# Kernel tuning notes

Measured on AMD Instinct MI355X. Metric: run time of the kernel, lower is better.

The kernel has to match this reference:

```python
import jax, jax.numpy as jnp
import numpy as np

B, T, D = 4, 8192, 512
N_LEVELS = 3
N_HEAD = 4
HEAD_DIM = D // N_HEAD
STRIDES = (8, 4, 4)
SEGS = (T // 8, T // 32, T // 128)  # 1024, 256, 64 segments per level
LN_EPS = 1e-5


def setup_inputs() -> dict:
    key = jax.random.key(0)
    ks = jax.random.split(key, 8)
    h_bytes = jax.random.normal(ks[0], (B, T, D), jnp.float32)
    def strided_boundaries(length, stride):
        b = np.zeros((B, length), np.int32)
        b[:, ::stride] = 1  # segment-start markers; first position always a boundary
        return jnp.asarray(b)
    b0 = strided_boundaries(T, STRIDES[0])
    b1 = strided_boundaries(SEGS[0], STRIDES[1])
    b2 = strided_boundaries(SEGS[1], STRIDES[2])
    s = 0.02
    return dict(
        h_bytes=h_bytes, b0=b0, b1=b1, b2=b2,
        mlp_ln_g=jnp.ones((N_LEVELS, D), jnp.float32),
        mlp_ln_b=jnp.zeros((N_LEVELS, D), jnp.float32),
        mlp_w1=jax.random.normal(ks[1], (N_LEVELS, D, 2 * D), jnp.float32) * s,
        mlp_b1=jnp.zeros((N_LEVELS, 2 * D), jnp.float32),
        mlp_w2=jax.random.normal(ks[2], (N_LEVELS, 2 * D, D), jnp.float32) * s,
        mlp_b2=jnp.zeros((N_LEVELS, D), jnp.float32),
        # 8 linears per cross-level block: bu_q,bu_k,bu_v,bu_out,td_q,td_k,td_v,td_out
        ca_w=jax.random.normal(ks[3], (N_LEVELS - 1, 8, D, D), jnp.float32) * s,
        ca_b=jnp.zeros((N_LEVELS - 1, 8, D), jnp.float32),
        ca_ln_g=jnp.ones((N_LEVELS - 1, 2, D), jnp.float32),  # [.,0]=bu_norm, [.,1]=td_norm
        ca_ln_b=jnp.zeros((N_LEVELS - 1, 2, D), jnp.float32),
    )


def _ln(x, g, b):
    mu = jnp.mean(x, axis=-1, keepdims=True)
    xc = x - mu
    var = jnp.mean(xc * xc, axis=-1, keepdims=True)
    return xc * jax.lax.rsqrt(var + LN_EPS) * g + b


def _mha(xq, xkv, Wq, Wk, Wv, Wo, bq, bk, bv, bo):
    Bq, Sq, _ = xq.shape
    Skv = xkv.shape[1]
    q = (xq @ Wq + bq).reshape(Bq, Sq, N_HEAD, HEAD_DIM)
    k = (xkv @ Wk + bk).reshape(Bq, Skv, N_HEAD, HEAD_DIM)
    v = (xkv @ Wv + bv).reshape(Bq, Skv, N_HEAD, HEAD_DIM)
    scores = jnp.einsum('bqhd,bkhd->bhqk', q, k) * (1.0 / (HEAD_DIM ** 0.5))
    att = jax.nn.softmax(scores, axis=-1)
    out = jnp.einsum('bhqk,bkhd->bqhd', att, v).reshape(Bq, Sq, D)
    return out @ Wo + bo


def _segment_mean_pool(x, seg_ids, n_seg):
    # x: [B, T, D], seg_ids: [B, T] in [0, n_seg)
    sums = jax.vmap(lambda xi, si: jax.ops.segment_sum(xi, si, num_segments=n_seg))(x, seg_ids)
    cnts = jax.vmap(lambda si: jax.ops.segment_sum(jnp.ones(si.shape, jnp.float32), si, num_segments=n_seg))(seg_ids)
    return sums / jnp.maximum(cnts, 1.0)[..., None]


def reference(h_bytes, b0, b1, b2, mlp_ln_g, mlp_ln_b, mlp_w1, mlp_b1, mlp_w2, mlp_b2, ca_w, ca_b, ca_ln_g, ca_ln_b):
    bounds = (b0, b1, b2)
    segs = []
    cur = h_bytes
    for lvl in range(N_LEVELS):
        seg_ids = jnp.cumsum(bounds[lvl], axis=1) - 1  # boundary marks segment start
        pooled = _segment_mean_pool(cur, seg_ids, SEGS[lvl])
        h = _ln(pooled, mlp_ln_g[lvl], mlp_ln_b[lvl])
        h = jax.nn.gelu(h @ mlp_w1[lvl] + mlp_b1[lvl], approximate=False)
        pooled = pooled + (h @ mlp_w2[lvl] + mlp_b2[lvl])
        segs.append(pooled)
        cur = pooled
    # top-down cross-level refinement
    for i in range(N_LEVELS - 2, -1, -1):
        fine, coarse = segs[i], segs[i + 1]
        fn = _ln(fine, ca_ln_g[i, 0], ca_ln_b[i, 0])
        fu = fine + _mha(fn, coarse, ca_w[i, 0], ca_w[i, 1], ca_w[i, 2], ca_w[i, 3],
                         ca_b[i, 0], ca_b[i, 1], ca_b[i, 2], ca_b[i, 3])
        cn = _ln(coarse, ca_ln_g[i, 1], ca_ln_b[i, 1])
        cu = coarse + _mha(cn, fu, ca_w[i, 4], ca_w[i, 5], ca_w[i, 6], ca_w[i, 7],
                           ca_b[i, 4], ca_b[i, 5], ca_b[i, 6], ca_b[i, 7])
        segs[i], segs[i + 1] = fu, cu
    return tuple(segs)
```

## Files before the change

### kernel.cpp

```cpp
#include <hip/hip_runtime.h>
#include <hip/hip_bf16.h>
#include <math.h>

#define NHEAD 4

typedef __attribute__((ext_vector_type(8))) short bf16x8;
typedef __attribute__((ext_vector_type(4))) float f32x4;
typedef unsigned short u16;

__device__ __forceinline__ u16 f2b(float f) {
  unsigned u = __float_as_uint(f);
  u = u + 0x7fffu + ((u >> 16) & 1u);
  return (u16)(u >> 16);
}
__device__ __forceinline__ float gelu_exact(float x) {
  return 0.5f * x * (1.0f + erff(x * 0.70710678118654752f));
}

__global__ __launch_bounds__(1024) void scan_bounds_kernel(
    const int* __restrict__ bnd, int* __restrict__ starts, int n, int nseg) {
  __shared__ int sums[1024];
  int row = blockIdx.x;
  const int* br = bnd + (size_t)row * n;
  int chunk = (n + 1023) / 1024;
  int t0 = threadIdx.x * chunk;
  int t1 = t0 + chunk; if (t1 > n) t1 = n;
  int s = 0;
  for (int t = t0; t < t1; ++t) s += br[t];
  sums[threadIdx.x] = s;
  __syncthreads();
  for (int off = 1; off < 1024; off <<= 1) {
    int v = (threadIdx.x >= off) ? sums[threadIdx.x - off] : 0;
    __syncthreads();
    sums[threadIdx.x] += v;
    __syncthreads();
  }
  int run = sums[threadIdx.x] - s;
  for (int t = t0; t < t1; ++t) {
    if (br[t]) { starts[(size_t)row * nseg + run] = t; ++run; }
  }
}

__global__ __launch_bounds__(128) void pool_kernel(
    const float* __restrict__ x, const int* __restrict__ starts,
    float* __restrict__ y, int Tin, int nseg) {
  int s = blockIdx.x, b = blockIdx.y;
  int st = starts[(size_t)b * nseg + s];
  int en = (s + 1 < nseg) ? starts[(size_t)b * nseg + s + 1] : Tin;
  const float* xb = x + (size_t)b * Tin * 512;
  int d = threadIdx.x * 4;
  float4 acc = make_float4(0.f, 0.f, 0.f, 0.f);
  for (int t = st; t < en; ++t) {
    float4 v = *(const float4*)(xb + (size_t)t * 512 + d);
    acc.x += v.x; acc.y += v.y; acc.z += v.z; acc.w += v.w;
  }
  int cnt = en - st; if (cnt < 1) cnt = 1;
  float inv = 1.0f / (float)cnt;
  *(float4*)(y + ((size_t)b * nseg + s) * 512 + d) =
      make_float4(acc.x * inv, acc.y * inv, acc.z * inv, acc.w * inv);
}

__global__ __launch_bounds__(256) void ln_kernel(
    const float* __restrict__ x, const float* __restrict__ g,
    const float* __restrict__ bt, u16* __restrict__ y, int ntok) {
  int wave = threadIdx.x >> 6, lane = threadIdx.x & 63;
  int tok = blockIdx.x * 4 + wave;
  if (tok >= ntok) return;
  const float* xr = x + (size_t)tok * 512;
  int d = lane * 8;
  float4 v0 = *(const float4*)(xr + d);
  float4 v1 = *(const float4*)(xr + d + 4);
  float s = v0.x + v0.y + v0.z + v0.w + v1.x + v1.y + v1.z + v1.w;
  #pragma unroll
  for (int off = 32; off; off >>= 1) s += __shfl_xor(s, off, 64);
  float mean = s * (1.0f / 512.0f);
  float a[8] = {v0.x-mean, v0.y-mean, v0.z-mean, v0.w-mean,
                v1.x-mean, v1.y-mean, v1.z-mean, v1.w-mean};
  float ss = 0.f;
  #pragma unroll
  for (int i = 0; i < 8; ++i) ss += a[i]*a[i];
  #pragma unroll
  for (int off = 32; off; off >>= 1) ss += __shfl_xor(ss, off, 64);
  float inv = rsqrtf(ss * (1.0f / 512.0f) + 1e-5f);
  float4 g0 = *(const float4*)(g + d), g1 = *(const float4*)(g + d + 4);
  float4 b0 = *(const float4*)(bt + d), b1 = *(const float4*)(bt + d + 4);
  float gg[8] = {g0.x,g0.y,g0.z,g0.w,g1.x,g1.y,g1.z,g1.w};
  float bb[8] = {b0.x,b0.y,b0.z,b0.w,b1.x,b1.y,b1.z,b1.w};
  union { u16 u[8]; uint4 v; } pk;
  #pragma unroll
  for (int i = 0; i < 8; ++i) pk.u[i] = f2b(a[i] * inv * gg[i] + bb[i]);
  *(uint4*)(y + (size_t)tok * 512 + d) = pk.v;
}

__global__ __launch_bounds__(256) void castbf_kernel(
    const float* __restrict__ x, u16* __restrict__ y, int n8) {
  int i = blockIdx.x * 256 + threadIdx.x;
  if (i >= n8) return;
  float4 v0 = *(const float4*)(x + (size_t)i * 8);
  float4 v1 = *(const float4*)(x + (size_t)i * 8 + 4);
  float a[8] = {v0.x,v0.y,v0.z,v0.w,v1.x,v1.y,v1.z,v1.w};
  union { u16 u[8]; uint4 v; } pk;
  #pragma unroll
  for (int j = 0; j < 8; ++j) pk.u[j] = f2b(a[j]);
  *(uint4*)(y + (size_t)i * 8) = pk.v;
}

__global__ __launch_bounds__(256) void wtrans_kernel(
    const float* __restrict__ W, u16* __restrict__ Wt, int K, int M) {
  __shared__ float tile[32][33];
  int m0 = blockIdx.x * 32, k0 = blockIdx.y * 32;
  const float* Wz = W + (size_t)blockIdx.z * K * M;
  u16* Wtz = Wt + (size_t)blockIdx.z * K * M;
  int x = threadIdx.x & 31, y = threadIdx.x >> 5;
  #pragma unroll
  for (int i = 0; i < 32; i += 8)
    tile[y + i][x] = Wz[(size_t)(k0 + y + i) * M + m0 + x];
  __syncthreads();
  #pragma unroll
  for (int i = 0; i < 32; i += 8)
    Wtz[(size_t)(m0 + y + i) * K + k0 + x] = f2b(tile[x][y + i]);
}

__global__ __launch_bounds__(256) void vtrans_kernel(
    const u16* __restrict__ vb, u16* __restrict__ vT, int Skv) {
  __shared__ u16 tile[32][33];
  int kv0 = blockIdx.x * 32, d0 = blockIdx.y * 32;
  int z = blockIdx.z, b = z >> 2, h = z & 3;
  const u16* src = vb + ((size_t)b * Skv) * 512 + h * 128;
  u16* dst = vT + (size_t)z * 128 * Skv;
  int x = threadIdx.x & 31, y = threadIdx.x >> 5;
  #pragma unroll
  for (int i = 0; i < 32; i += 8)
    tile[y + i][x] = src[(size_t)(kv0 + y + i) * 512 + d0 + x];
  __syncthreads();
  #pragma unroll
  for (int i = 0; i < 32; i += 8)
    dst[(size_t)(d0 + y + i) * Skv + kv0 + x] = tile[x][y + i];
}

__global__ __launch_bounds__(256) void softmax_kernel(
    const float* __restrict__ S, u16* __restrict__ P, int L) {
  int wave = threadIdx.x >> 6, lane = threadIdx.x & 63;
  int row = blockIdx.x * 4 + wave;
  const float* sr = S + (size_t)row * L;
  u16* pr = P + (size_t)row * L;
  const float scale = 0.08838834764831845f;
  float mx = -1e30f;
  for (int j = lane; j < L; j += 64) mx = fmaxf(mx, sr[j]);
  #pragma unroll
  for (int off = 32; off; off >>= 1) mx = fmaxf(mx, __shfl_xor(mx, off, 64));
  float e[16];
  int cnt = L >> 6;
  float sum = 0.f;
  for (int c = 0; c < cnt; ++c) {
    e[c] = __expf((sr[lane + (c << 6)] - mx) * scale);
    sum += e[c];
  }
  #pragma unroll
  for (int off = 32; off; off >>= 1) sum += __shfl_xor(sum, off, 64);
  float inv = 1.0f / sum;
  for (int c = 0; c < cnt; ++c) pr[lane + (c << 6)] = f2b(e[c] * inv);
}

__device__ __forceinline__ void mfma_core(
    const u16* __restrict__ A, int lda, const u16* __restrict__ Wt, int ldw,
    int K, u16* AsB, u16* WsB, f32x4 acc[2][2]) {
  int t = threadIdx.x;
  int lane = t & 63, wave = t >> 6;
  int wr = (wave >> 1) * 32, wc = (wave & 1) * 32;
  int lrow = t >> 3;
  int lseg = t & 7;
  int swz = (lseg * 16) ^ ((lrow & 7) << 4);
  const u16* Ap0 = A + (size_t)lrow * lda + lseg * 8;
  const u16* Ap1 = Ap0 + (size_t)32 * lda;
  const u16* Wp0 = Wt + (size_t)lrow * ldw + lseg * 8;
  const u16* Wp1 = Wp0 + (size_t)32 * ldw;
  for (int k0 = 0; k0 < K; k0 += 64) {
    uint4 a0 = *(const uint4*)(Ap0 + k0);
    uint4 a1 = *(const uint4*)(Ap1 + k0);
    uint4 w0 = *(const uint4*)(Wp0 + k0);
    uint4 w1 = *(const uint4*)(Wp1 + k0);
    __syncthreads();
    *(uint4*)((char*)AsB + lrow * 128 + swz) = a0;
    *(uint4*)((char*)AsB + (lrow + 32) * 128 + swz) = a1;
    *(uint4*)((char*)WsB + lrow * 128 + swz) = w0;
    *(uint4*)((char*)WsB + (lrow + 32) * 128 + swz) = w1;
    __syncthreads();
    #pragma unroll
    for (int ks = 0; ks < 2; ++ks) {
      bf16x8 af[2], bfr[2];
      #pragma unroll
      for (int mi = 0; mi < 2; ++mi) {
        int row = wr + mi * 16 + (lane & 15);
        int cb = (ks * 64 + ((lane >> 4) << 4)) ^ ((row & 7) << 4);
        af[mi] = *(const bf16x8*)((const char*)AsB + row * 128 + cb);
      }
      #pragma unroll
      for (int ni = 0; ni < 2; ++ni) {
        int row = wc + ni * 16 + (lane & 15);
        int cb = (ks * 64 + ((lane >> 4) << 4)) ^ ((row & 7) << 4);
        bfr[ni] = *(const bf16x8*)((const char*)WsB + row * 128 + cb);
      }
      #pragma unroll
      for (int mi = 0; mi < 2; ++mi)
        #pragma unroll
        for (int ni = 0; ni < 2; ++ni)
          acc[mi][ni] = __builtin_amdgcn_mfma_f32_16x16x32_bf16(
              af[mi], bfr[ni], acc[mi][ni], 0, 0, 0);
    }
  }
}

__global__ __launch_bounds__(256) void gemm_k(
    const u16* __restrict__ A, int lda, const u16* __restrict__ Wt, int ldw,
    int K, const float* __restrict__ bias, float* __restrict__ Cf,
    u16* __restrict__ Cb, int ldc, int flags) {
  __shared__ u16 As[4096], Ws[4096];
  int n0 = blockIdx.y * 64, m0 = blockIdx.x * 64;
  f32x4 acc[2][2];
  #pragma unroll
  for (int i = 0; i < 2; ++i)
    #pragma unroll
    for (int j = 0; j < 2; ++j) acc[i][j] = (f32x4){0.f, 0.f, 0.f, 0.f};
  mfma_core(A + (size_t)n0 * lda, lda, Wt + (size_t)m0 * ldw, ldw, K, As, Ws, acc);
  int lane = threadIdx.x & 63, wave = threadIdx.x >> 6;
  int wr = (wave >> 1) * 32, wc = (wave & 1) * 32;
  #pragma unroll
  for (int mi = 0; mi < 2; ++mi) {
    #pragma unroll
    for (int ni = 0; ni < 2; ++ni) {
      int col = m0 + wc + ni * 16 + (lane & 15);
      float bv = bias[col];
      #pragma unroll
      for (int j = 0; j < 4; ++j) {
        int row = n0 + wr + mi * 16 + ((lane >> 4) << 2) + j;
        float v = acc[mi][ni][j] + bv;
        if (flags & 1) v = gelu_exact(v);
        size_t idx = (size_t)row * ldc + col;
        if (flags & 2) v += Cf[idx];
        if (flags & 4) Cf[idx] = v;
        if (flags & 8) Cb[idx] = f2b(v);
      }
    }
  }
}

__global__ __launch_bounds__(256) void scores_k(
    const u16* __restrict__ Qb, const u16* __restrict__ Kb,
    float* __restrict__ S, int Sq, int Skv) {
  __shared__ u16 As[4096], Ws[4096];
  int z = blockIdx.z, b = z >> 2, h = z & 3;
  int n0 = blockIdx.y * 64, m0 = blockIdx.x * 64;
  const u16* Ap = Qb + ((size_t)b * Sq + n0) * 512 + h * 128;
  const u16* Wp = Kb + ((size_t)b * Skv + m0) * 512 + h * 128;
  f32x4 acc[2][2];
  #pragma unroll
  for (int i = 0; i < 2; ++i)
    #pragma unroll
    for (int j = 0; j < 2; ++j) acc[i][j] = (f32x4){0.f, 0.f, 0.f, 0.f};
  mfma_core(Ap, 512, Wp, 512, 128, As, Ws, acc);
  float* Sz = S + (size_t)z * Sq * Skv;
  int lane = threadIdx.x & 63, wave = threadIdx.x >> 6;
  int wr = (wave >> 1) * 32, wc = (wave & 1) * 32;
  #pragma unroll
  for (int mi = 0; mi < 2; ++mi)
    #pragma unroll
    for (int ni = 0; ni < 2; ++ni) {
      int col = m0 + wc + ni * 16 + (lane & 15);
      #pragma unroll
      for (int j = 0; j < 4; ++j) {
        int row = n0 + wr + mi * 16 + ((lane >> 4) << 2) + j;
        Sz[(size_t)row * Skv + col] = acc[mi][ni][j];
      }
    }
}

__global__ __launch_bounds__(256) void pv_k(
    const u16* __restrict__ P, const u16* __restrict__ vT,
    u16* __restrict__ O, int Sq, int Skv) {
  __shared__ u16 As[4096], Ws[4096];
  int z = blockIdx.z, b = z >> 2, h = z & 3;
  int n0 = blockIdx.y * 64, m0 = blockIdx.x * 64;
  const u16* Ap = P + (size_t)z * Sq * Skv + (size_t)n0 * Skv;
  const u16* Wp = vT + (size_t)z * 128 * Skv + (size_t)m0 * Skv;
  f32x4 acc[2][2];
  #pragma unroll
  for (int i = 0; i < 2; ++i)
    #pragma unroll
    for (int j = 0; j < 2; ++j) acc[i][j] = (f32x4){0.f, 0.f, 0.f, 0.f};
  mfma_core(Ap, Skv, Wp, Skv, Skv, As, Ws, acc);
  int lane = threadIdx.x & 63, wave = threadIdx.x >> 6;
  int wr = (wave >> 1) * 32, wc = (wave & 1) * 32;
  #pragma unroll
  for (int mi = 0; mi < 2; ++mi)
    #pragma unroll
    for (int ni = 0; ni < 2; ++ni) {
      int col = m0 + wc + ni * 16 + (lane & 15);
      #pragma unroll
      for (int j = 0; j < 4; ++j) {
        int row = n0 + wr + mi * 16 + ((lane >> 4) << 2) + j;
        O[((size_t)b * Sq + row) * 512 + h * 128 + col] = f2b(acc[mi][ni][j]);
      }
    }
}

extern "C" void kernel_launch(void* const* d_in, const int* in_sizes, int n_in,
                              void* d_out, int out_size, void* d_ws, size_t ws_size,
                              hipStream_t stream) {
  (void)in_sizes; (void)n_in; (void)out_size; (void)ws_size;
  const float* h_bytes  = (const float*)d_in[0];
  const int*   b0       = (const int*)d_in[1];
  const int*   b1       = (const int*)d_in[2];
  const int*   b2       = (const int*)d_in[3];
  const float* mlp_ln_g = (const float*)d_in[4];
  const float* mlp_ln_b = (const float*)d_in[5];
  const float* mlp_w1   = (const float*)d_in[6];
  const float* mlp_b1   = (const float*)d_in[7];
  const float* mlp_w2   = (const float*)d_in[8];
  const float* mlp_b2   = (const float*)d_in[9];
  const float* ca_w     = (const float*)d_in[10];
  const float* ca_b     = (const float*)d_in[11];
  const float* ca_ln_g  = (const float*)d_in[12];
  const float* ca_ln_b  = (const float*)d_in[13];

  float* out0 = (float*)d_out;
  float* out1 = out0 + 4 * 1024 * 512;
  float* out2 = out1 + 4 * 256 * 512;

  char* wsb = (char*)d_ws;
  u16* w1t = (u16*)wsb;
  u16* w2t = w1t + 3 * 524288;
  u16* cat = w2t + 3 * 524288;
  u16*   lnbuf = (u16*)(wsb + (14u << 20));
  u16*   hbuf  = (u16*)(wsb + (18u << 20));
  u16*   qb    = (u16*)(wsb + (18u << 20));
  u16*   kb    = (u16*)(wsb + (22u << 20));
  u16*   Pbuf  = (u16*)(wsb + (18u << 20));
  u16*   vT    = (u16*)(wsb + (26u << 20));
  u16*   vb    = (u16*)(wsb + (30u << 20));
  u16*   ccbf  = (u16*)(wsb + (34u << 20));
  float* Sbuf  = (float*)(wsb + (30u << 20));
  u16*   abuf  = (u16*)(wsb + (46u << 20));
  int* starts0 = (int*)(wsb + (50u << 20));
  int* starts1 = starts0 + 4096;
  int* starts2 = starts1 + 1024;

  wtrans_kernel<<<dim3(32, 16, 3), 256, 0, stream>>>(mlp_w1, w1t, 512, 1024);
  wtrans_kernel<<<dim3(16, 32, 3), 256, 0, stream>>>(mlp_w2, w2t, 1024, 512);
  wtrans_kernel<<<dim3(16, 16, 16), 256, 0, stream>>>(ca_w, cat, 512, 512);

  scan_bounds_kernel<<<4, 1024, 0, stream>>>(b0, starts0, 8192, 1024);
  scan_bounds_kernel<<<4, 1024, 0, stream>>>(b1, starts1, 1024, 256);
  scan_bounds_kernel<<<4, 1024, 0, stream>>>(b2, starts2, 256, 64);

  auto mlp = [&](float* X, int Ntok, int lvl) {
    ln_kernel<<<Ntok / 4, 256, 0, stream>>>(X, mlp_ln_g + lvl * 512,
                                            mlp_ln_b + lvl * 512, lnbuf, Ntok);
    gemm_k<<<dim3(16, Ntok / 64), 256, 0, stream>>>(
        lnbuf, 512, w1t + (size_t)lvl * 524288, 512, 512,
        mlp_b1 + lvl * 1024, nullptr, hbuf, 1024, 1 | 8);
    gemm_k<<<dim3(8, Ntok / 64), 256, 0, stream>>>(
        hbuf, 1024, w2t + (size_t)lvl * 524288, 1024, 1024,
        mlp_b2 + lvl * 512, X, nullptr, 512, 2 | 4);
  };
  pool_kernel<<<dim3(1024, 4), 128, 0, stream>>>(h_bytes, starts0, out0, 8192, 1024);
  mlp(out0, 4096, 0);
  pool_kernel<<<dim3(256, 4), 128, 0, stream>>>(out0, starts1, out1, 1024, 256);
  mlp(out1, 1024, 1);
  pool_kernel<<<dim3(64, 4), 128, 0, stream>>>(out1, starts2, out2, 256, 64);
  mlp(out2, 256, 2);

  auto cross = [&](int i, float* F, float* Cc, int nf, int nc) {
    u16* cw = cat + (size_t)i * 8 * 262144;
    const float* bb = ca_b + (size_t)i * 8 * 512;
    const float* lg = ca_ln_g + (size_t)i * 2 * 512;
    const float* lb = ca_ln_b + (size_t)i * 2 * 512;
    int Nf = 4 * nf, Nc = 4 * nc;
    ln_kernel<<<Nf / 4, 256, 0, stream>>>(F, lg, lb, lnbuf, Nf);
    gemm_k<<<dim3(8, Nf / 64), 256, 0, stream>>>(lnbuf, 512, cw, 512, 512,
                                                 bb, nullptr, qb, 512, 8);
    castbf_kernel<<<Nc / 4, 256, 0, stream>>>(Cc, ccbf, Nc * 64);
    gemm_k<<<dim3(8, Nc / 64), 256, 0, stream>>>(ccbf, 512, cw + 262144, 512, 512,
                                                 bb + 512, nullptr, kb, 512, 8);
    gemm_k<<<dim3(8, Nc / 64), 256, 0, stream>>>(ccbf, 512, cw + 2 * 262144, 512, 512,
                                                 bb + 1024, nullptr, vb, 512, 8);
    vtrans_kernel<<<dim3(nc / 32, 4, 16), 256, 0, stream>>>(vb, vT, nc);
    scores_k<<<dim3(nc / 64, nf / 64, 16), 256, 0, stream>>>(qb, kb, Sbuf, nf, nc);
    softmax_kernel<<<16 * nf / 4, 256, 0, stream>>>(Sbuf, Pbuf, nc);
    pv_k<<<dim3(2, nf / 64, 16), 256, 0, stream>>>(Pbuf, vT, abuf, nf, nc);
    gemm_k<<<dim3(8, Nf / 64), 256, 0, stream>>>(abuf, 512, cw + 3 * 262144, 512, 512,
                                                 bb + 3 * 512, F, nullptr, 512, 2 | 4);
    ln_kernel<<<Nc / 4, 256, 0, stream>>>(Cc, lg + 512, lb + 512, lnbuf, Nc);
    gemm_k<<<dim3(8, Nc / 64), 256, 0, stream>>>(lnbuf, 512, cw + 4 * 262144, 512, 512,
                                                 bb + 4 * 512, nullptr, qb, 512, 8);
    castbf_kernel<<<Nf / 4, 256, 0, stream>>>(F, ccbf, Nf * 64);
    gemm_k<<<dim3(8, Nf / 64), 256, 0, stream>>>(ccbf, 512, cw + 5 * 262144, 512, 512,
                                                 bb + 5 * 512, nullptr, kb, 512, 8);
    gemm_k<<<dim3(8, Nf / 64), 256, 0, stream>>>(ccbf, 512, cw + 6 * 262144, 512, 512,
                                                 bb + 6 * 512, nullptr, vb, 512, 8);
    vtrans_kernel<<<dim3(nf / 32, 4, 16), 256, 0, stream>>>(vb, vT, nf);
    scores_k<<<dim3(nf / 64, nc / 64, 16), 256, 0, stream>>>(qb, kb, Sbuf, nc, nf);
    softmax_kernel<<<16 * nc / 4, 256, 0, stream>>>(Sbuf, Pbuf, nf);
    pv_k<<<dim3(2, nc / 64, 16), 256, 0, stream>>>(Pbuf, vT, abuf, nc, nf);
    gemm_k<<<dim3(8, Nc / 64), 256, 0, stream>>>(abuf, 512, cw + 7 * 262144, 512, 512,
                                                 bb + 7 * 512, Cc, nullptr, 512, 2 | 4);
  };
  cross(1, out1, out2, 256, 64);
  cross(0, out0, out1, 1024, 256);
}
```

Before: 516.7 us.

## Fuse attention into flash kernel, merge launches, fuse pool+LN, prefetch GEMM tiles

Replaces the separate scores, softmax and PV kernels with a single fused attention kernel that keeps the scores on chip. The softmax skips the max subtraction and normalises once at the end. The pool and LayerNorm steps are fused into one kernel. The three weight-transpose launches and three scan launches are each merged into one. K and V projections are merged into a single wider GEMM, and the GEMM epilogues write bf16 mirrors so the cast kernels are no longer needed. The GEMM main loop gains register prefetch of the next K tile. Together these cut launches and HBM traffic for the score matrices, but dropping the max subtraction in softmax risks overflow when logits are large.

```diff
diff --git a/kernel.cpp b/kernel.cpp
--- a/kernel.cpp
+++ b/kernel.cpp
@@ -1,8 +1,6 @@
 #include <hip/hip_runtime.h>
 #include <hip/hip_bf16.h>
 #include <math.h>
-
-#define NHEAD 4
 
 typedef __attribute__((ext_vector_type(8))) short bf16x8;
 typedef __attribute__((ext_vector_type(4))) float f32x4;
@@ -17,14 +15,20 @@
   return 0.5f * x * (1.0f + erff(x * 0.70710678118654752f));
 }
 
-__global__ __launch_bounds__(1024) void scan_bounds_kernel(
-    const int* __restrict__ bnd, int* __restrict__ starts, int n, int nseg) {
+__global__ __launch_bounds__(1024) void scan_all_k(
+    const int* __restrict__ b0, const int* __restrict__ b1,
+    const int* __restrict__ b2, int* __restrict__ starts) {
   __shared__ int sums[1024];
-  int row = blockIdx.x;
-  const int* br = bnd + (size_t)row * n;
+  int lvl = blockIdx.y, row = blockIdx.x;
+  const int* bp = (lvl == 0) ? b0 : (lvl == 1) ? b1 : b2;
+  int n = (lvl == 0) ? 8192 : (lvl == 1) ? 1024 : 256;
+  int nseg = (lvl == 0) ? 1024 : (lvl == 1) ? 256 : 64;
+  int* sp = starts + ((lvl == 0) ? 0 : (lvl == 1) ? 4096 : 5120);
+  const int* br = bp + (size_t)row * n;
   int chunk = (n + 1023) / 1024;
   int t0 = threadIdx.x * chunk;
   int t1 = t0 + chunk; if (t1 > n) t1 = n;
+  if (t0 > n) t0 = n;
   int s = 0;
   for (int t = t0; t < t1; ++t) s += br[t];
   sums[threadIdx.x] = s;
@@ -37,27 +41,85 @@
   }
   int run = sums[threadIdx.x] - s;
   for (int t = t0; t < t1; ++t) {
-    if (br[t]) { starts[(size_t)row * nseg + run] = t; ++run; }
-  }
-}
-
-__global__ __launch_bounds__(128) void pool_kernel(
+    if (br[t]) { sp[(size_t)row * nseg + run] = t; ++run; }
+  }
+}
+
+__global__ __launch_bounds__(256) void wtrans_all_k(
+    const float* __restrict__ w1, const float* __restrict__ w2,
+    const float* __restrict__ ca, u16* __restrict__ w1t,
+    u16* __restrict__ w2t, u16* __restrict__ cat) {
+  __shared__ float tile[32][33];
+  int z = blockIdx.x;
+  const float* W; u16* Wt; int K, M, m0, k0;
+  if (z < 1536) {
+    int mat = z >> 9, tl = z & 511;
+    W = w1 + (size_t)mat * 524288; Wt = w1t + (size_t)mat * 524288;
+    K = 512; M = 1024; m0 = (tl & 31) * 32; k0 = (tl >> 5) * 32;
+  } else if (z < 3072) {
+    z -= 1536; int mat = z >> 9, tl = z & 511;
+    W = w2 + (size_t)mat * 524288; Wt = w2t + (size_t)mat * 524288;
+    K = 1024; M = 512; m0 = (tl & 15) * 32; k0 = (tl >> 4) * 32;
+  } else {
+    z -= 3072; int mat = z >> 8, tl = z & 255;
+    W = ca + (size_t)mat * 262144; Wt = cat + (size_t)mat * 262144;
+    K = 512; M = 512; m0 = (tl & 15) * 32; k0 = (tl >> 4) * 32;
+  }
+  int x = threadIdx.x & 31, y = threadIdx.x >> 5;
+  #pragma unroll
+  for (int i = 0; i < 32; i += 8)
+    tile[y + i][x] = W[(size_t)(k0 + y + i) * M + m0 + x];
+  __syncthreads();
+  #pragma unroll
+  for (int i = 0; i < 32; i += 8)
+    Wt[(size_t)(m0 + y + i) * K + k0 + x] = f2b(tile[x][y + i]);
+}
+
+__global__ __launch_bounds__(256) void pool_ln_k(
     const float* __restrict__ x, const int* __restrict__ starts,
-    float* __restrict__ y, int Tin, int nseg) {
-  int s = blockIdx.x, b = blockIdx.y;
+    float* __restrict__ pooled, const float* __restrict__ g,
+    const float* __restrict__ bt, u16* __restrict__ lnout,
+    int Tin, int nseg) {
+  int wv = threadIdx.x >> 6, lane = threadIdx.x & 63;
+  int s = blockIdx.x * 4 + wv, b = blockIdx.y;
   int st = starts[(size_t)b * nseg + s];
   int en = (s + 1 < nseg) ? starts[(size_t)b * nseg + s + 1] : Tin;
-  const float* xb = x + (size_t)b * Tin * 512;
-  int d = threadIdx.x * 4;
-  float4 acc = make_float4(0.f, 0.f, 0.f, 0.f);
+  const float* xb = x + ((size_t)b * Tin) * 512;
+  int d = lane * 8;
+  float a[8] = {0.f,0.f,0.f,0.f,0.f,0.f,0.f,0.f};
   for (int t = st; t < en; ++t) {
-    float4 v = *(const float4*)(xb + (size_t)t * 512 + d);
-    acc.x += v.x; acc.y += v.y; acc.z += v.z; acc.w += v.w;
+    const float* row = xb + (size_t)t * 512 + d;
+    float4 v0 = *(const float4*)row;
+    float4 v1 = *(const float4*)(row + 4);
+    a[0]+=v0.x; a[1]+=v0.y; a[2]+=v0.z; a[3]+=v0.w;
+    a[4]+=v1.x; a[5]+=v1.y; a[6]+=v1.z; a[7]+=v1.w;
   }
   int cnt = en - st; if (cnt < 1) cnt = 1;
-  float inv = 1.0f / (float)cnt;
-  *(float4*)(y + ((size_t)b * nseg + s) * 512 + d) =
-      make_float4(acc.x * inv, acc.y * inv, acc.z * inv, acc.w * inv);
+  float ic = 1.0f / (float)cnt;
+  #pragma unroll
+  for (int i = 0; i < 8; ++i) a[i] *= ic;
+  int tok = b * nseg + s;
+  float* pr = pooled + (size_t)tok * 512 + d;
+  *(float4*)pr = make_float4(a[0], a[1], a[2], a[3]);
+  *(float4*)(pr + 4) = make_float4(a[4], a[5], a[6], a[7]);
+  float sm = a[0]+a[1]+a[2]+a[3]+a[4]+a[5]+a[6]+a[7];
+  #pragma unroll
+  for (int off = 32; off; off >>= 1) sm += __shfl_xor(sm, off, 64);
+  float mean = sm * (1.0f / 512.0f);
+  float ss = 0.f;
+  #pragma unroll
+  for (int i = 0; i < 8; ++i) { a[i] -= mean; ss += a[i]*a[i]; }
+  #pragma unroll
+  for (int off = 32; off; off >>= 1) ss += __shfl_xor(ss, off, 64);
+  float inv = rsqrtf(ss * (1.0f / 512.0f) + 1e-5f);
+  float4 g0 = *(const float4*)(g + d), g1 = *(const float4*)(g + d + 4);
+  float4 b0 = *(const float4*)(bt + d), b1 = *(const float4*)(bt + d + 4);
+  float gg[8] = {g0.x,g0.y,g0.z,g0.w,g1.x,g1.y,g1.z,g1.w};
+  float bb[8] = {b0.x,b0.y,b0.z,b0.w,b1.x,b1.y,b1.z,b1.w};
+  union { u16 u[8]; uint4 v; } pk;
+  #pragma unroll
+  for (int i = 0; i < 8; ++i) pk.u[i] = f2b(a[i] * inv * gg[i] + bb[i]);
+  *(uint4*)(lnout + (size_t)tok * 512 + d) = pk.v;
 }
 
 __global__ __launch_bounds__(256) void ln_kernel(
@@ -92,74 +154,21 @@
   *(uint4*)(y + (size_t)tok * 512 + d) = pk.v;
 }
 
-__global__ __launch_bounds__(256) void castbf_kernel(
-    const float* __restrict__ x, u16* __restrict__ y, int n8) {
-  int i = blockIdx.x * 256 + threadIdx.x;
-  if (i >= n8) return;
-  float4 v0 = *(const float4*)(x + (size_t)i * 8);
-  float4 v1 = *(const float4*)(x + (size_t)i * 8 + 4);
-  float a[8] = {v0.x,v0.y,v0.z,v0.w,v1.x,v1.y,v1.z,v1.w};
-  union { u16 u[8]; uint4 v; } pk;
-  #pragma unroll
-  for (int j = 0; j < 8; ++j) pk.u[j] = f2b(a[j]);
-  *(uint4*)(y + (size_t)i * 8) = pk.v;
-}
-
-__global__ __launch_bounds__(256) void wtrans_kernel(
-    const float* __restrict__ W, u16* __restrict__ Wt, int K, int M) {
-  __shared__ float tile[32][33];
-  int m0 = blockIdx.x * 32, k0 = blockIdx.y * 32;
-  const float* Wz = W + (size_t)blockIdx.z * K * M;
-  u16* Wtz = Wt + (size_t)blockIdx.z * K * M;
-  int x = threadIdx.x & 31, y = threadIdx.x >> 5;
-  #pragma unroll
-  for (int i = 0; i < 32; i += 8)
-    tile[y + i][x] = Wz[(size_t)(k0 + y + i) * M + m0 + x];
-  __syncthreads();
-  #pragma unroll
-  for (int i = 0; i < 32; i += 8)
-    Wtz[(size_t)(m0 + y + i) * K + k0 + x] = f2b(tile[x][y + i]);
-}
-
 __global__ __launch_bounds__(256) void vtrans_kernel(
-    const u16* __restrict__ vb, u16* __restrict__ vT, int Skv) {
+    const u16* __restrict__ vsrc, int lds_, u16* __restrict__ vT, int Skv) {
   __shared__ u16 tile[32][33];
   int kv0 = blockIdx.x * 32, d0 = blockIdx.y * 32;
   int z = blockIdx.z, b = z >> 2, h = z & 3;
-  const u16* src = vb + ((size_t)b * Skv) * 512 + h * 128;
+  const u16* src = vsrc + ((size_t)b * Skv) * lds_ + h * 128;
   u16* dst = vT + (size_t)z * 128 * Skv;
   int x = threadIdx.x & 31, y = threadIdx.x >> 5;
   #pragma unroll
   for (int i = 0; i < 32; i += 8)
-    tile[y + i][x] = src[(size_t)(kv0 + y + i) * 512 + d0 + x];
+    tile[y + i][x] = src[(size_t)(kv0 + y + i) * lds_ + d0 + x];
   __syncthreads();
   #pragma unroll
   for (int i = 0; i < 32; i += 8)
     dst[(size_t)(d0 + y + i) * Skv + kv0 + x] = tile[x][y + i];
-}
-
-__global__ __launch_bounds__(256) void softmax_kernel(
-    const float* __restrict__ S, u16* __restrict__ P, int L) {
-  int wave = threadIdx.x >> 6, lane = threadIdx.x & 63;
-  int row = blockIdx.x * 4 + wave;
-  const float* sr = S + (size_t)row * L;
-  u16* pr = P + (size_t)row * L;
-  const float scale = 0.08838834764831845f;
-  float mx = -1e30f;
-  for (int j = lane; j < L; j += 64) mx = fmaxf(mx, sr[j]);
-  #pragma unroll
-  for (int off = 32; off; off >>= 1) mx = fmaxf(mx, __shfl_xor(mx, off, 64));
-  float e[16];
-  int cnt = L >> 6;
-  float sum = 0.f;
-  for (int c = 0; c < cnt; ++c) {
-    e[c] = __expf((sr[lane + (c << 6)] - mx) * scale);
-    sum += e[c];
-  }
-  #pragma unroll
-  for (int off = 32; off; off >>= 1) sum += __shfl_xor(sum, off, 64);
-  float inv = 1.0f / sum;
-  for (int c = 0; c < cnt; ++c) pr[lane + (c << 6)] = f2b(e[c] * inv);
 }
 
 __device__ __forceinline__ void mfma_core(
@@ -175,17 +184,23 @@
   const u16* Ap1 = Ap0 + (size_t)32 * lda;
   const u16* Wp0 = Wt + (size_t)lrow * ldw + lseg * 8;
   const u16* Wp1 = Wp0 + (size_t)32 * ldw;
+  uint4 a0 = *(const uint4*)(Ap0);
+  uint4 a1 = *(const uint4*)(Ap1);
+  uint4 w0 = *(const uint4*)(Wp0);
+  uint4 w1 = *(const uint4*)(Wp1);
   for (int k0 = 0; k0 < K; k0 += 64) {
-    uint4 a0 = *(const uint4*)(Ap0 + k0);
-    uint4 a1 = *(const uint4*)(Ap1 + k0);
-    uint4 w0 = *(const uint4*)(Wp0 + k0);
-    uint4 w1 = *(const uint4*)(Wp1 + k0);
     __syncthreads();
     *(uint4*)((char*)AsB + lrow * 128 + swz) = a0;
     *(uint4*)((char*)AsB + (lrow + 32) * 128 + swz) = a1;
     *(uint4*)((char*)WsB + lrow * 128 + swz) = w0;
     *(uint4*)((char*)WsB + (lrow + 32) * 128 + swz) = w1;
     __syncthreads();
+    if (k0 + 64 < K) {
+      a0 = *(const uint4*)(Ap0 + k0 + 64);
+      a1 = *(const uint4*)(Ap1 + k0 + 64);
+      w0 = *(const uint4*)(Wp0 + k0 + 64);
+      w1 = *(const uint4*)(Wp1 + k0 + 64);
+    }
     #pragma unroll
     for (int ks = 0; ks < 2; ++ks) {
       bf16x8 af[2], bfr[2];
@@ -245,63 +260,93 @@
   }
 }
 
-__global__ __launch_bounds__(256) void scores_k(
-    const u16* __restrict__ Qb, const u16* __restrict__ Kb,
-    float* __restrict__ S, int Sq, int Skv) {
-  __shared__ u16 As[4096], Ws[4096];
-  int z = blockIdx.z, b = z >> 2, h = z & 3;
-  int n0 = blockIdx.y * 64, m0 = blockIdx.x * 64;
-  const u16* Ap = Qb + ((size_t)b * Sq + n0) * 512 + h * 128;
-  const u16* Wp = Kb + ((size_t)b * Skv + m0) * 512 + h * 128;
-  f32x4 acc[2][2];
-  #pragma unroll
-  for (int i = 0; i < 2; ++i)
-    #pragma unroll
-    for (int j = 0; j < 2; ++j) acc[i][j] = (f32x4){0.f, 0.f, 0.f, 0.f};
-  mfma_core(Ap, 512, Wp, 512, 128, As, Ws, acc);
-  float* Sz = S + (size_t)z * Sq * Skv;
-  int lane = threadIdx.x & 63, wave = threadIdx.x >> 6;
-  int wr = (wave >> 1) * 32, wc = (wave & 1) * 32;
-  #pragma unroll
-  for (int mi = 0; mi < 2; ++mi)
-    #pragma unroll
-    for (int ni = 0; ni < 2; ++ni) {
-      int col = m0 + wc + ni * 16 + (lane & 15);
-      #pragma unroll
-      for (int j = 0; j < 4; ++j) {
-        int row = n0 + wr + mi * 16 + ((lane >> 4) << 2) + j;
-        Sz[(size_t)row * Skv + col] = acc[mi][ni][j];
+__global__ __launch_bounds__(256) void fattn_k(
+    const u16* __restrict__ Q, int ldq, const u16* __restrict__ KV, int ldkv,
+    const u16* __restrict__ vT, u16* __restrict__ O, int ldo,
+    int Sq, int Skv) {
+  __shared__ u16 Ks[64 * 128];
+  __shared__ u16 Vs[128 * 64];
+  __shared__ u16 Ps[4][16 * 64];
+  int z = blockIdx.y, b = z >> 2, h = z & 3;
+  int t = threadIdx.x, lane = t & 63, w = t >> 6;
+  int g = lane >> 4, ql = lane & 15;
+  int q0 = blockIdx.x * 64;
+  const float scale = 0.08838834764831845f;
+  bf16x8 qf[4];
+  {
+    const u16* qp = Q + ((size_t)(b * Sq + q0 + 16 * w + ql)) * ldq + h * 128 + g * 8;
+    #pragma unroll
+    for (int ks = 0; ks < 4; ++ks) qf[ks] = *(const bf16x8*)(qp + 32 * ks);
+  }
+  f32x4 o[8];
+  #pragma unroll
+  for (int i = 0; i < 8; ++i) o[i] = (f32x4){0.f, 0.f, 0.f, 0.f};
+  float lsum = 0.f;
+  for (int kv0 = 0; kv0 < Skv; kv0 += 64) {
+    uint4 kreg[4], vreg[4];
+    const u16* kbase = KV + ((size_t)(b * Skv + kv0)) * ldkv + h * 128;
+    const u16* vbase = vT + (size_t)z * 128 * Skv + kv0;
+    #pragma unroll
+    for (int i = 0; i < 4; ++i) {
+      int idx = t + i * 256;
+      kreg[i] = *(const uint4*)(kbase + (size_t)(idx >> 4) * ldkv + (idx & 15) * 8);
+      vreg[i] = *(const uint4*)(vbase + (size_t)(idx >> 3) * Skv + (idx & 7) * 8);
+    }
+    __syncthreads();
+    #pragma unroll
+    for (int i = 0; i < 4; ++i) {
+      int idx = t + i * 256;
+      int kr = idx >> 4, kss = idx & 15;
+      *(uint4*)((char*)Ks + kr * 256 + (((kss ^ (kr & 7))) << 4)) = kreg[i];
+      int vd = idx >> 3, vs = idx & 7;
+      *(uint4*)((char*)Vs + vd * 128 + (((vs ^ (vd & 7))) << 4)) = vreg[i];
+    }
+    __syncthreads();
+    float rs = 0.f;
+    #pragma unroll
+    for (int kvt = 0; kvt < 4; ++kvt) {
+      f32x4 acc = (f32x4){0.f, 0.f, 0.f, 0.f};
+      int row = kvt * 16 + ql;
+      #pragma unroll
+      for (int ks = 0; ks < 4; ++ks) {
+        int seg = (4 * ks + g) ^ (row & 7);
+        bf16x8 kf = *(const bf16x8*)((const char*)Ks + row * 256 + seg * 16);
+        acc = __builtin_amdgcn_mfma_f32_16x16x32_bf16(kf, qf[ks], acc, 0, 0, 0);
       }
-    }
-}
-
-__global__ __launch_bounds__(256) void pv_k(
-    const u16* __restrict__ P, const u16* __restrict__ vT,
-    u16* __restrict__ O, int Sq, int Skv) {
-  __shared__ u16 As[4096], Ws[4096];
-  int z = blockIdx.z, b = z >> 2, h = z & 3;
-  int n0 = blockIdx.y * 64, m0 = blockIdx.x * 64;
-  const u16* Ap = P + (size_t)z * Sq * Skv + (size_t)n0 * Skv;
-  const u16* Wp = vT + (size_t)z * 128 * Skv + (size_t)m0 * Skv;
-  f32x4 acc[2][2];
-  #pragma unroll
-  for (int i = 0; i < 2; ++i)
-    #pragma unroll
-    for (int j = 0; j < 2; ++j) acc[i][j] = (f32x4){0.f, 0.f, 0.f, 0.f};
-  mfma_core(Ap, Skv, Wp, Skv, Skv, As, Ws, acc);
-  int lane = threadIdx.x & 63, wave = threadIdx.x >> 6;
-  int wr = (wave >> 1) * 32, wc = (wave & 1) * 32;
-  #pragma unroll
-  for (int mi = 0; mi < 2; ++mi)
-    #pragma unroll
-    for (int ni = 0; ni < 2; ++ni) {
-      int col = m0 + wc + ni * 16 + (lane & 15);
-      #pragma unroll
-      for (int j = 0; j < 4; ++j) {
-        int row = n0 + wr + mi * 16 + ((lane >> 4) << 2) + j;
-        O[((size_t)b * Sq + row) * 512 + h * 128 + col] = f2b(acc[mi][ni][j]);
+      float e0 = __expf(acc[0] * scale), e1 = __expf(acc[1] * scale);
+      float e2 = __expf(acc[2] * scale), e3 = __expf(acc[3] * scale);
+      rs += e0 + e1 + e2 + e3;
+      unsigned lo = (unsigned)f2b(e0) | ((unsigned)f2b(e1) << 16);
+      unsigned hi = (unsigned)f2b(e2) | ((unsigned)f2b(e3) << 16);
+      int slot = (2 * kvt + (g >> 1)) ^ (ql & 7);
+      *(uint2*)((char*)Ps[w] + ql * 128 + slot * 16 + 8 * (g & 1)) =
+          make_uint2(lo, hi);
+    }
+    rs += __shfl_xor(rs, 16, 64);
+    rs += __shfl_xor(rs, 32, 64);
+    lsum += rs;
+    #pragma unroll
+    for (int kh = 0; kh < 2; ++kh) {
+      int slot = (4 * kh + g) ^ (ql & 7);
+      bf16x8 pa = *(const bf16x8*)((const char*)Ps[w] + ql * 128 + slot * 16);
+      #pragma unroll
+      for (int dt = 0; dt < 8; ++dt) {
+        int dr = dt * 16 + ql;
+        bf16x8 vf = *(const bf16x8*)((const char*)Vs + dr * 128 +
+                                     (((4 * kh + g) ^ (dr & 7)) << 4));
+        o[dt] = __builtin_amdgcn_mfma_f32_16x16x32_bf16(pa, vf, o[dt], 0, 0, 0);
       }
     }
+  }
+  float linv[4];
+  #pragma unroll
+  for (int r = 0; r < 4; ++r) linv[r] = 1.0f / __shfl(lsum, 4 * g + r, 64);
+  u16* ob = O + ((size_t)(b * Sq + q0 + 16 * w)) * ldo + h * 128;
+  #pragma unroll
+  for (int dt = 0; dt < 8; ++dt)
+    #pragma unroll
+    for (int r = 0; r < 4; ++r)
+      ob[(size_t)(4 * g + r) * ldo + dt * 16 + ql] = f2b(o[dt][r] * linv[r]);
 }
 
 extern "C" void kernel_launch(void* const* d_in, const int* in_sizes, int n_in,
@@ -328,49 +373,46 @@
   float* out2 = out1 + 4 * 256 * 512;
 
   char* wsb = (char*)d_ws;
-  u16* w1t = (u16*)wsb;
-  u16* w2t = w1t + 3 * 524288;
-  u16* cat = w2t + 3 * 524288;
-  u16*   lnbuf = (u16*)(wsb + (14u << 20));
-  u16*   hbuf  = (u16*)(wsb + (18u << 20));
-  u16*   qb    = (u16*)(wsb + (18u << 20));
-  u16*   kb    = (u16*)(wsb + (22u << 20));
-  u16*   Pbuf  = (u16*)(wsb + (18u << 20));
-  u16*   vT    = (u16*)(wsb + (26u << 20));
-  u16*   vb    = (u16*)(wsb + (30u << 20));
-  u16*   ccbf  = (u16*)(wsb + (34u << 20));
-  float* Sbuf  = (float*)(wsb + (30u << 20));
-  u16*   abuf  = (u16*)(wsb + (46u << 20));
-  int* starts0 = (int*)(wsb + (50u << 20));
-  int* starts1 = starts0 + 4096;
-  int* starts2 = starts1 + 1024;
-
-  wtrans_kernel<<<dim3(32, 16, 3), 256, 0, stream>>>(mlp_w1, w1t, 512, 1024);
-  wtrans_kernel<<<dim3(16, 32, 3), 256, 0, stream>>>(mlp_w2, w2t, 1024, 512);
-  wtrans_kernel<<<dim3(16, 16, 16), 256, 0, stream>>>(ca_w, cat, 512, 512);
-
-  scan_bounds_kernel<<<4, 1024, 0, stream>>>(b0, starts0, 8192, 1024);
-  scan_bounds_kernel<<<4, 1024, 0, stream>>>(b1, starts1, 1024, 256);
-  scan_bounds_kernel<<<4, 1024, 0, stream>>>(b2, starts2, 256, 64);
-
-  auto mlp = [&](float* X, int Ntok, int lvl) {
-    ln_kernel<<<Ntok / 4, 256, 0, stream>>>(X, mlp_ln_g + lvl * 512,
-                                            mlp_ln_b + lvl * 512, lnbuf, Ntok);
+  const size_t MB = 1048576;
+  u16* w1t   = (u16*)(wsb + 0 * MB);
+  u16* w2t   = (u16*)(wsb + 3 * MB);
+  u16* cat   = (u16*)(wsb + 6 * MB);
+  u16* m0b   = (u16*)(wsb + 14 * MB);
+  u16* m1b   = (u16*)(wsb + 18 * MB);
+  u16* m2b   = (u16*)(wsb + 19 * MB);
+  u16* lnbuf = (u16*)(wsb + 20 * MB);
+  u16* hbuf  = (u16*)(wsb + 24 * MB);
+  u16* qb    = (u16*)(wsb + 32 * MB);
+  u16* kvbuf = (u16*)(wsb + 36 * MB);
+  u16* vT    = (u16*)(wsb + 44 * MB);
+  u16* abuf  = (u16*)(wsb + 48 * MB);
+  int* starts  = (int*)(wsb + 52 * MB);
+  int* starts0 = starts;
+  int* starts1 = starts + 4096;
+  int* starts2 = starts + 5120;
+
+  wtrans_all_k<<<7168, 256, 0, stream>>>(mlp_w1, mlp_w2, ca_w, w1t, w2t, cat);
+  scan_all_k<<<dim3(4, 3), 1024, 0, stream>>>(b0, b1, b2, starts);
+
+  auto mlp = [&](float* X, u16* mir, int Ntok, int lvl) {
     gemm_k<<<dim3(16, Ntok / 64), 256, 0, stream>>>(
         lnbuf, 512, w1t + (size_t)lvl * 524288, 512, 512,
         mlp_b1 + lvl * 1024, nullptr, hbuf, 1024, 1 | 8);
     gemm_k<<<dim3(8, Ntok / 64), 256, 0, stream>>>(
         hbuf, 1024, w2t + (size_t)lvl * 524288, 1024, 1024,
-        mlp_b2 + lvl * 512, X, nullptr, 512, 2 | 4);
+        mlp_b2 + lvl * 512, X, mir, 512, 2 | 4 | 8);
   };
-  pool_kernel<<<dim3(1024, 4), 128, 0, stream>>>(h_bytes, starts0, out0, 8192, 1024);
-  mlp(out0, 4096, 0);
-  pool_kernel<<<dim3(256, 4), 128, 0, stream>>>(out0, starts1, out1, 1024, 256);
-  mlp(out1, 1024, 1);
-  pool_kernel<<<dim3(64, 4), 128, 0, stream>>>(out1, starts2, out2, 256, 64);
-  mlp(out2, 256, 2);
-
-  auto cross = [&](int i, float* F, float* Cc, int nf, int nc) {
+  pool_ln_k<<<dim3(256, 4), 256, 0, stream>>>(h_bytes, starts0, out0,
+      mlp_ln_g, mlp_ln_b, lnbuf, 8192, 1024);
+  mlp(out0, m0b, 4096, 0);
+  pool_ln_k<<<dim3(64, 4), 256, 0, stream>>>(out0, starts1, out1,
+      mlp_ln_g + 512, mlp_ln_b + 512, lnbuf, 1024, 256);
+  mlp(out1, m1b, 1024, 1);
+  pool_ln_k<<<dim3(16, 4), 256, 0, stream>>>(out1, starts2, out2,
+      mlp_ln_g + 1024, mlp_ln_b + 1024, lnbuf, 256, 64);
+  mlp(out2, m2b, 256, 2);
+
+  auto cross = [&](int i, float* F, u16* mf, float* Cc, u16* mc, int nf, int nc) {
     u16* cw = cat + (size_t)i * 8 * 262144;
     const float* bb = ca_b + (size_t)i * 8 * 512;
     const float* lg = ca_ln_g + (size_t)i * 2 * 512;
@@ -378,33 +420,25 @@
     int Nf = 4 * nf, Nc = 4 * nc;
     ln_kernel<<<Nf / 4, 256, 0, stream>>>(F, lg, lb, lnbuf, Nf);
     gemm_k<<<dim3(8, Nf / 64), 256, 0, stream>>>(lnbuf, 512, cw, 512, 512,
-                                                 bb, nullptr, qb, 512, 8);
-    castbf_kernel<<<Nc / 4, 256, 0, stream>>>(Cc, ccbf, Nc * 64);
-    gemm_k<<<dim3(8, Nc / 64), 256, 0, stream>>>(ccbf, 512, cw + 262144, 512, 512,
-                                                 bb + 512, nullptr, kb, 512, 8);
-    gemm_k<<<dim3(8, Nc / 64), 256, 0, stream>>>(ccbf, 512, cw + 2 * 262144, 512, 512,
-                                                 bb + 1024, nullptr, vb, 512, 8);
-    vtrans_kernel<<<dim3(nc / 32, 4, 16), 256, 0, stream>>>(vb, vT, nc);
-    scores_k<<<dim3(nc / 64, nf / 64, 16), 256, 0, stream>>>(qb, kb, Sbuf, nf, nc);
-    softmax_kernel<<<16 * nf / 4, 256, 0, stream>>>(Sbuf, Pbuf, nc);
-    pv_k<<<dim3(2, nf / 64, 16), 256, 0, stream>>>(Pbuf, vT, abuf, nf, nc);
+        bb, nullptr, qb, 512, 8);
+    gemm_k<<<dim3(16, Nc / 64), 256, 0, stream>>>(mc, 512, cw + 262144, 512, 512,
+        bb + 512, nullptr, kvbuf, 1024, 8);
+    vtrans_kernel<<<dim3(nc / 32, 4, 16), 256, 0, stream>>>(kvbuf + 512, 1024, vT, nc);
+    fattn_k<<<dim3(nf / 64, 16), 256, 0, stream>>>(qb, 512, kvbuf, 1024, vT,
+        abuf, 512, nf, nc);
     gemm_k<<<dim3(8, Nf / 64), 256, 0, stream>>>(abuf, 512, cw + 3 * 262144, 512, 512,
-                                                 bb + 3 * 512, F, nullptr, 512, 2 | 4);
+        bb + 3 * 512, F, mf, 512, 2 | 4 | 8);
     ln_kernel<<<Nc / 4, 256, 0, stream>>>(Cc, lg + 512, lb + 512, lnbuf, Nc);
     gemm_k<<<dim3(8, Nc / 64), 256, 0, stream>>>(lnbuf, 512, cw + 4 * 262144, 512, 512,
-                                                 bb + 4 * 512, nullptr, qb, 512, 8);
-    castbf_kernel<<<Nf / 4, 256, 0, stream>>>(F, ccbf, Nf * 64);
-    gemm_k<<<dim3(8, Nf / 64), 256, 0, stream>>>(ccbf, 512, cw + 5 * 262144, 512, 512,
-                                                 bb + 5 * 512, nullptr, kb, 512, 8);
-    gemm_k<<<dim3(8, Nf / 64), 256, 0, stream>>>(ccbf, 512, cw + 6 * 262144, 512, 512,
-                                                 bb + 6 * 512, nullptr, vb, 512, 8);
-    vtrans_kernel<<<dim3(nf / 32, 4, 16), 256, 0, stream>>>(vb, vT, nf);
-    scores_k<<<dim3(nf / 64, nc / 64, 16), 256, 0, stream>>>(qb, kb, Sbuf, nc, nf);
-    softmax_kernel<<<16 * nc / 4, 256, 0, stream>>>(Sbuf, Pbuf, nf);
-    pv_k<<<dim3(2, nc / 64, 16), 256, 0, stream>>>(Pbuf, vT, abuf, nc, nf);
+        bb + 4 * 512, nullptr, qb, 512, 8);
+    gemm_k<<<dim3(16, Nf / 64), 256, 0, stream>>>(mf, 512, cw + 5 * 262144, 512, 512,
+        bb + 5 * 512, nullptr, kvbuf, 1024, 8);
+    vtrans_kernel<<<dim3(nf / 32, 4, 16), 256, 0, stream>>>(kvbuf + 512, 1024, vT, nf);
+    fattn_k<<<dim3(nc / 64, 16), 256, 0, stream>>>(qb, 512, kvbuf, 1024, vT,
+        abuf, 512, nc, nf);
     gemm_k<<<dim3(8, Nc / 64), 256, 0, stream>>>(abuf, 512, cw + 7 * 262144, 512, 512,
-                                                 bb + 7 * 512, Cc, nullptr, 512, 2 | 4);
+        bb + 7 * 512, Cc, mc, 512, 2 | 4 | 8);
   };
-  cross(1, out1, out2, 256, 64);
-  cross(0, out0, out1, 1024, 256);
-}
+  cross(1, out1, m1b, out2, m2b, 256, 64);
+  cross(0, out0, m0b, out1, m1b, 1024, 256);
+}
```

Measured after the change: 522.2 us. No clear change (+1.1%).
